# Optimization experiments

Hardware: AMD Instinct MI355X
Metric: run time of the kernel (lower is better)

## Reference

```python
import jax, jax.numpy as jnp
import numpy as np

N_NODES = 20000
N_EDGES = 320000
IN_DIM = 128
HID = 64
HEADS = 4
NEG_SLOPE = 0.2  # PyG GATConv default


def _glorot(key, shape):
    fan_in, fan_out = shape[0], shape[-1]
    lim = jnp.sqrt(6.0 / (fan_in + fan_out))
    return jax.random.uniform(key, shape, jnp.float32, -lim, lim)


def setup_inputs() -> dict:
    key = jax.random.key(0)
    ks = jax.random.split(key, 16)
    x = jax.random.normal(ks[0], (N_NODES, IN_DIM), jnp.float32)
    edge_index = jax.random.randint(ks[1], (2, N_EDGES), 0, N_NODES, dtype=jnp.int64)
    # layer 1: in=128 -> heads=4, out=64, concat
    W1 = _glorot(ks[2], (IN_DIM, HEADS * HID))
    a_src1 = _glorot(ks[3], (HEADS, HID))
    a_dst1 = _glorot(ks[4], (HEADS, HID))
    b1 = jnp.zeros((HEADS * HID,), jnp.float32)
    # layer 2: in=256 -> heads=4, out=64, concat
    W2 = _glorot(ks[5], (HEADS * HID, HEADS * HID))
    a_src2 = _glorot(ks[6], (HEADS, HID))
    a_dst2 = _glorot(ks[7], (HEADS, HID))
    b2 = jnp.zeros((HEADS * HID,), jnp.float32)
    # layer 3: in=256 -> heads=1, out=1, mean (concat=False)
    W3 = _glorot(ks[8], (HEADS * HID, 1))
    a_src3 = _glorot(ks[9], (1, 1))
    a_dst3 = _glorot(ks[10], (1, 1))
    b3 = jnp.zeros((1,), jnp.float32)
    return {
        "x": x, "edge_index": edge_index,
        "W1": W1, "a_src1": a_src1, "a_dst1": a_dst1, "b1": b1,
        "W2": W2, "a_src2": a_src2, "a_dst2": a_dst2, "b2": b2,
        "W3": W3, "a_src3": a_src3, "a_dst3": a_dst3, "b3": b3,
    }


def gat_conv(x, src, dst, W, a_src, a_dst, b, heads, out_c, concat):
    """PyG GATConv (add_self_loops already applied to src/dst)."""
    n = x.shape[0]
    h = (x @ W).reshape(n, heads, out_c)            # [N,H,C]
    alpha_s = jnp.sum(h * a_src, axis=-1)           # [N,H]
    alpha_d = jnp.sum(h * a_dst, axis=-1)           # [N,H]
    e = jax.nn.leaky_relu(alpha_s[src] + alpha_d[dst], NEG_SLOPE)  # [E,H]
    # segment softmax over incoming edges of each destination node
    e_max = jax.ops.segment_max(e, dst, num_segments=n)            # [N,H]
    ex = jnp.exp(e - e_max[dst])                                   # [E,H]
    denom = jax.ops.segment_sum(ex, dst, num_segments=n)           # [N,H]
    alpha = ex / denom[dst]                                        # [E,H]
    msg = h[src] * alpha[:, :, None]                               # [E,H,C]
    out = jax.ops.segment_sum(msg, dst, num_segments=n)            # [N,H,C]
    if concat:
        out = out.reshape(n, heads * out_c)
    else:
        out = out.mean(axis=1)
    return out + b


def reference(x, edge_index, W1, a_src1, a_dst1, b1, W2, a_src2, a_dst2, b2,
              W3, a_src3, a_dst3, b3):
    n = x.shape[0]
    loops = jnp.arange(n, dtype=edge_index.dtype)
    src = jnp.concatenate([edge_index[0], loops])
    dst = jnp.concatenate([edge_index[1], loops])
    h = jax.nn.elu(gat_conv(x, src, dst, W1, a_src1, a_dst1, b1, HEADS, HID, True))
    # dropout is identity in eval mode
    h = jax.nn.elu(gat_conv(h, src, dst, W2, a_src2, a_dst2, b2, HEADS, HID, True))
    h = gat_conv(h, src, dst, W3, a_src3, a_dst3, b3, 1, 1, False)
    return h.reshape(-1)
```

## Files before the change

kernel.cpp:

```cpp
#include <hip/hip_runtime.h>
#include <hip/hip_bf16.h>
#include <cmath>

#define N_NODESC 20000
#define E_RAW    320000
#define E_TOTC   340000
#define HEADSC   4
#define FC       256
#define NEG_SLOPE 0.2f
#define MAXD     512

typedef __attribute__((ext_vector_type(8))) short short8v;
typedef __attribute__((ext_vector_type(4))) float f32x4;

__device__ __forceinline__ int dstOf(const int* ei, int e) {
  return (e < E_RAW) ? ei[E_RAW + e] : (e - E_RAW);
}
__device__ __forceinline__ int srcOf(const int* ei, int e) {
  return (e < E_RAW) ? ei[e] : (e - E_RAW);
}
__device__ __forceinline__ float lrelu(float v) { return v > 0.f ? v : NEG_SLOPE * v; }

__device__ __forceinline__ unsigned short f2bf(float f) {
  __hip_bfloat16 h = __float2bfloat16(f);
  return reinterpret_cast<unsigned short&>(h);
}
__device__ __forceinline__ float bf2f(unsigned short u) {
  return __uint_as_float(((unsigned int)u) << 16);
}

__global__ void mega_prep(const float* __restrict__ x,
                          unsigned short* __restrict__ xhi, unsigned short* __restrict__ xlo,
                          const float* __restrict__ W1,
                          unsigned short* __restrict__ w1hi, unsigned short* __restrict__ w1lo,
                          const float* __restrict__ W2,
                          unsigned short* __restrict__ w2hi, unsigned short* __restrict__ w2lo,
                          int* __restrict__ deg) {
  const int bid = blockIdx.x, t = threadIdx.x;
  if (bid < 10000) {
    int i = bid * 256 + t;
    float v = x[i];
    unsigned short hh = f2bf(v);
    xhi[i] = hh; xlo[i] = f2bf(v - bf2f(hh));
  } else if (bid < 10128) {
    int idx = (bid - 10000) * 256 + t;
    int c = idx >> 7, k = idx & 127;
    float v = W1[k * FC + c];
    unsigned short hh = f2bf(v);
    w1hi[c * 128 + k] = hh; w1lo[c * 128 + k] = f2bf(v - bf2f(hh));
  } else if (bid < 10384) {
    int idx = (bid - 10128) * 256 + t;
    int c = idx >> 8, k = idx & 255;
    float v = W2[k * FC + c];
    unsigned short hh = f2bf(v);
    w2hi[c * 256 + k] = hh; w2lo[c * 256 + k] = f2bf(v - bf2f(hh));
  } else {
    int i = (bid - 10384) * 256 + t;
    if (i < N_NODESC) deg[i] = 0;
  }
}

template<int K>
__global__ void __launch_bounds__(256) mfma_gemm(
    const unsigned short* __restrict__ Ahi, const unsigned short* __restrict__ Alo,
    const unsigned short* __restrict__ WhiT, const unsigned short* __restrict__ WloT,
    const float* __restrict__ a_src, const float* __restrict__ a_dst,
    unsigned short* __restrict__ hb, float* __restrict__ as, float* __restrict__ ad) {
  __shared__ float asred[64][4];
  __shared__ float adred[64][4];
  const int t = threadIdx.x;
  const int w = t >> 6, l = t & 63;
  const int n0 = blockIdx.x * 64;
  const int r16 = l & 15;
  const int kq = l >> 4;
  const int col0 = w * 64;

  f32x4 acc[4][4];
#pragma unroll
  for (int rt = 0; rt < 4; ++rt)
#pragma unroll
    for (int ct = 0; ct < 4; ++ct) acc[rt][ct] = f32x4{0.f, 0.f, 0.f, 0.f};

  long arow[4];
#pragma unroll
  for (int rt = 0; rt < 4; ++rt) {
    int r = n0 + rt * 16 + r16;
    if (r >= N_NODESC) r = N_NODESC - 1;
    arow[rt] = (long)r * K;
  }

  for (int ks = 0; ks < K; ks += 32) {
    const int kb = ks + kq * 8;
    short8v aHi[4], aLo[4];
#pragma unroll
    for (int rt = 0; rt < 4; ++rt) {
      aHi[rt] = *(const short8v*)(Ahi + arow[rt] + kb);
      aLo[rt] = *(const short8v*)(Alo + arow[rt] + kb);
    }
#pragma unroll
    for (int ct = 0; ct < 4; ++ct) {
      const long wrow = (long)(col0 + ct * 16 + r16) * K + kb;
      short8v wHi = *(const short8v*)(WhiT + wrow);
      short8v wLo = *(const short8v*)(WloT + wrow);
#pragma unroll
      for (int rt = 0; rt < 4; ++rt) {
        acc[rt][ct] = __builtin_amdgcn_mfma_f32_16x16x32_bf16(aHi[rt], wHi, acc[rt][ct], 0, 0, 0);
        acc[rt][ct] = __builtin_amdgcn_mfma_f32_16x16x32_bf16(aHi[rt], wLo, acc[rt][ct], 0, 0, 0);
        acc[rt][ct] = __builtin_amdgcn_mfma_f32_16x16x32_bf16(aLo[rt], wHi, acc[rt][ct], 0, 0, 0);
      }
    }
  }

  float asv[4], adv[4];
#pragma unroll
  for (int ct = 0; ct < 4; ++ct) {
    int c = col0 + ct * 16 + r16;
    asv[ct] = a_src[c];
    adv[ct] = a_dst[c];
  }
#pragma unroll
  for (int rt = 0; rt < 4; ++rt) {
#pragma unroll
    for (int j = 0; j < 4; ++j) {
      const int r = rt * 16 + kq * 4 + j;
      const int g = n0 + r;
      if (g < N_NODESC) {
#pragma unroll
        for (int ct = 0; ct < 4; ++ct)
          hb[(long)g * FC + col0 + ct * 16 + r16] = f2bf(acc[rt][ct][j]);
      }
      float ps = acc[rt][0][j] * asv[0] + acc[rt][1][j] * asv[1]
               + acc[rt][2][j] * asv[2] + acc[rt][3][j] * asv[3];
      float pd = acc[rt][0][j] * adv[0] + acc[rt][1][j] * adv[1]
               + acc[rt][2][j] * adv[2] + acc[rt][3][j] * adv[3];
      for (int off = 8; off; off >>= 1) {
        ps += __shfl_down(ps, off, 16);
        pd += __shfl_down(pd, off, 16);
      }
      if (r16 == 0) {
        asred[r][w] = ps;
        adred[r][w] = pd;
      }
    }
  }
  __syncthreads();
  {
    const int rr = t >> 2, hh = t & 3;
    const int g = n0 + rr;
    if (g < N_NODESC) {
      as[(long)g * HEADSC + hh] = asred[rr][hh];
      ad[(long)g * HEADSC + hh] = adred[rr][hh];
    }
  }
}

__global__ void gemm3_kernel(const unsigned short* __restrict__ act_hi,
                             const unsigned short* __restrict__ act_lo,
                             const float* __restrict__ W3,
                             const float* __restrict__ asc, const float* __restrict__ adc,
                             float* __restrict__ h3, float* __restrict__ as,
                             float* __restrict__ ad) {
  const int n = blockIdx.x;
  const int t = threadIdx.x;
  float a = bf2f(act_hi[(long)n * FC + t]) + bf2f(act_lo[(long)n * FC + t]);
  float v = a * W3[t];
  for (int off = 32; off; off >>= 1) v += __shfl_down(v, off, 64);
  __shared__ float red[4];
  if ((t & 63) == 0) red[t >> 6] = v;
  __syncthreads();
  if (t == 0) {
    float s = red[0] + red[1] + red[2] + red[3];
    h3[n] = s;
    as[n] = s * asc[0];
    ad[n] = s * adc[0];
  }
}

__global__ void deg_count(const int* __restrict__ ei, int* __restrict__ deg) {
  int e = blockIdx.x * 256 + threadIdx.x;
  if (e >= E_TOTC) return;
  atomicAdd(&deg[dstOf(ei, e)], 1);
}

__global__ void scan_kernel(const int* __restrict__ deg, int* __restrict__ row_ptr,
                            int* __restrict__ cursor) {
  __shared__ int partial[1024];
  const int t = threadIdx.x;
  const int PER = (N_NODESC + 1023) / 1024;
  const int base = t * PER;
  int s = 0;
  for (int i = 0; i < PER; ++i) {
    int idx = base + i;
    if (idx < N_NODESC) s += deg[idx];
  }
  partial[t] = s;
  __syncthreads();
  for (int off = 1; off < 1024; off <<= 1) {
    int v = (t >= off) ? partial[t - off] : 0;
    __syncthreads();
    partial[t] += v;
    __syncthreads();
  }
  int run = (t == 0) ? 0 : partial[t - 1];
  for (int i = 0; i < PER; ++i) {
    int idx = base + i;
    if (idx < N_NODESC) {
      row_ptr[idx] = run;
      cursor[idx]  = run;
      run += deg[idx];
    }
  }
  if (t == 1023) row_ptr[N_NODESC] = run;
}

__global__ void fill_kernel(const int* __restrict__ ei, int* __restrict__ cursor,
                            int* __restrict__ col_src) {
  int e = blockIdx.x * 256 + threadIdx.x;
  if (e >= E_TOTC) return;
  int d = dstOf(ei, e);
  int pos = atomicAdd(&cursor[d], 1);
  col_src[pos] = srcOf(ei, e);
}

template<bool ELU>
__global__ void __launch_bounds__(128) fused_sa(
    const int* __restrict__ row_ptr, const int* __restrict__ col_src,
    const float4* __restrict__ as4, const float4* __restrict__ ad4,
    const unsigned short* __restrict__ hb, const float* __restrict__ b,
    unsigned short* __restrict__ out_hi, unsigned short* __restrict__ out_lo) {
  const int d = blockIdx.x;
  const int t = threadIdx.x;
  const int l = t & 63, wv = t >> 6;
  const int j0 = row_ptr[d], j1 = row_ptr[d + 1];
  const int deg = j1 - j0;
  __shared__ float4 wbuf[MAXD];
  __shared__ float4 xred[2];
  const float4 adv = ad4[d];

  float4 mx = float4{-INFINITY, -INFINITY, -INFINITY, -INFINITY};
  for (int j = j0 + t; j < j1; j += 128) {
    float4 a = as4[col_src[j]];
    float4 v;
    v.x = lrelu(a.x + adv.x); v.y = lrelu(a.y + adv.y);
    v.z = lrelu(a.z + adv.z); v.w = lrelu(a.w + adv.w);
    int jj = j - j0;
    if (jj < MAXD) wbuf[jj] = v;
    mx.x = fmaxf(mx.x, v.x); mx.y = fmaxf(mx.y, v.y);
    mx.z = fmaxf(mx.z, v.z); mx.w = fmaxf(mx.w, v.w);
  }
  for (int off = 32; off; off >>= 1) {
    mx.x = fmaxf(mx.x, __shfl_xor(mx.x, off, 64));
    mx.y = fmaxf(mx.y, __shfl_xor(mx.y, off, 64));
    mx.z = fmaxf(mx.z, __shfl_xor(mx.z, off, 64));
    mx.w = fmaxf(mx.w, __shfl_xor(mx.w, off, 64));
  }
  if (l == 0) xred[wv] = mx;
  __syncthreads();
  {
    float4 m0 = xred[0], m1 = xred[1];
    mx.x = fmaxf(m0.x, m1.x); mx.y = fmaxf(m0.y, m1.y);
    mx.z = fmaxf(m0.z, m1.z); mx.w = fmaxf(m0.w, m1.w);
  }
  __syncthreads();

  float4 sm = float4{0.f, 0.f, 0.f, 0.f};
  for (int j = j0 + t; j < j1; j += 128) {
    int jj = j - j0;
    float4 v;
    if (jj < MAXD) v = wbuf[jj];
    else {
      float4 a = as4[col_src[j]];
      v.x = lrelu(a.x + adv.x); v.y = lrelu(a.y + adv.y);
      v.z = lrelu(a.z + adv.z); v.w = lrelu(a.w + adv.w);
    }
    float4 e;
    e.x = expf(v.x - mx.x); e.y = expf(v.y - mx.y);
    e.z = expf(v.z - mx.z); e.w = expf(v.w - mx.w);
    if (jj < MAXD) wbuf[jj] = e;
    sm.x += e.x; sm.y += e.y; sm.z += e.z; sm.w += e.w;
  }
  for (int off = 32; off; off >>= 1) {
    sm.x += __shfl_xor(sm.x, off, 64);
    sm.y += __shfl_xor(sm.y, off, 64);
    sm.z += __shfl_xor(sm.z, off, 64);
    sm.w += __shfl_xor(sm.w, off, 64);
  }
  if (l == 0) xred[wv] = sm;
  __syncthreads();

  const int h = t >> 5;
  float st0, mxh, advh;
  {
    float4 s0 = xred[0], s1 = xred[1];
    float sx = s0.x + s1.x, sy = s0.y + s1.y, sz = s0.z + s1.z, sw = s0.w + s1.w;
    st0  = (h == 0) ? sx : (h == 1) ? sy : (h == 2) ? sz : sw;
    mxh  = (h == 0) ? mx.x : (h == 1) ? mx.y : (h == 2) ? mx.z : mx.w;
    advh = (h == 0) ? adv.x : (h == 1) ? adv.y : (h == 2) ? adv.z : adv.w;
  }
  const float dnh = 1.f / st0;

  const float* wlds = (const float*)wbuf;
  const ushort2* hb2 = (const ushort2*)hb;
  float a0 = 0.f, a1 = 0.f;
  if (deg <= MAXD) {
    int j = j0;
    for (; j + 8 <= j1; j += 8) {
      int     s[8];
      ushort2 v[8];
      float   w[8];
#pragma unroll
      for (int u = 0; u < 8; ++u) s[u] = col_src[j + u];
#pragma unroll
      for (int u = 0; u < 8; ++u) v[u] = hb2[(long)s[u] * 128 + t];
#pragma unroll
      for (int u = 0; u < 8; ++u) w[u] = wlds[(j + u - j0) * 4 + h];
#pragma unroll
      for (int u = 0; u < 8; ++u) {
        a0 = fmaf(w[u], bf2f(v[u].x), a0);
        a1 = fmaf(w[u], bf2f(v[u].y), a1);
      }
    }
    for (; j < j1; ++j) {
      ushort2 v = hb2[(long)col_src[j] * 128 + t];
      float w = wlds[(j - j0) * 4 + h];
      a0 = fmaf(w, bf2f(v.x), a0);
      a1 = fmaf(w, bf2f(v.y), a1);
    }
  } else {
    const float* asf = (const float*)as4;
    for (int j = j0; j < j1; ++j) {
      int s = col_src[j];
      float e = expf(lrelu(asf[s * 4 + h] + advh) - mxh);
      ushort2 v = hb2[(long)s * 128 + t];
      a0 = fmaf(e, bf2f(v.x), a0);
      a1 = fmaf(e, bf2f(v.y), a1);
    }
  }
  float o0 = a0 * dnh + b[2 * t];
  float o1 = a1 * dnh + b[2 * t + 1];
  if (ELU) {
    o0 = o0 > 0.f ? o0 : expm1f(o0);
    o1 = o1 > 0.f ? o1 : expm1f(o1);
  }
  ushort2 hi, lo;
  hi.x = f2bf(o0); lo.x = f2bf(o0 - bf2f(hi.x));
  hi.y = f2bf(o1); lo.y = f2bf(o1 - bf2f(hi.y));
  ((ushort2*)out_hi)[(long)d * 128 + t] = hi;
  ((ushort2*)out_lo)[(long)d * 128 + t] = lo;
}

__global__ void __launch_bounds__(256) fused_sa3(
    const int* __restrict__ row_ptr, const int* __restrict__ col_src,
    const float* __restrict__ as, const float* __restrict__ ad,
    const float* __restrict__ h3, const float* __restrict__ b3,
    float* __restrict__ out) {
  const int wv = threadIdx.x >> 6, l = threadIdx.x & 63;
  const int d = blockIdx.x * 4 + wv;
  if (d >= N_NODESC) return;
  const int j0 = row_ptr[d], j1 = row_ptr[d + 1];
  const float adv = ad[d];
  float mx = -INFINITY;
  for (int j = j0 + l; j < j1; j += 64)
    mx = fmaxf(mx, lrelu(as[col_src[j]] + adv));
  for (int off = 32; off; off >>= 1) mx = fmaxf(mx, __shfl_xor(mx, off, 64));
  float sm = 0.f, acc = 0.f;
  for (int j = j0 + l; j < j1; j += 64) {
    int s = col_src[j];
    float e = expf(lrelu(as[s] + adv) - mx);
    sm += e;
    acc = fmaf(e, h3[s], acc);
  }
  for (int off = 32; off; off >>= 1) {
    sm  += __shfl_xor(sm, off, 64);
    acc += __shfl_xor(acc, off, 64);
  }
  if (l == 0) out[d] = acc / sm + b3[0];
}

extern "C" void kernel_launch(void* const* d_in, const int* in_sizes, int n_in,
                              void* d_out, int out_size, void* d_ws, size_t ws_size,
                              hipStream_t stream) {
  const float* x    = (const float*)d_in[0];
  const int*   ei   = (const int*)d_in[1];
  const float* W1   = (const float*)d_in[2];
  const float* as1  = (const float*)d_in[3];
  const float* ad1  = (const float*)d_in[4];
  const float* b1   = (const float*)d_in[5];
  const float* W2   = (const float*)d_in[6];
  const float* as2  = (const float*)d_in[7];
  const float* ad2  = (const float*)d_in[8];
  const float* b2   = (const float*)d_in[9];
  const float* W3   = (const float*)d_in[10];
  const float* as3  = (const float*)d_in[11];
  const float* ad3  = (const float*)d_in[12];
  const float* b3   = (const float*)d_in[13];
  float* out = (float*)d_out;

  float* ws = (float*)d_ws;
  size_t off = 0;
  float* wAs   = ws + off; off += (size_t)N_NODESC * HEADSC;
  float* wAd   = ws + off; off += (size_t)N_NODESC * HEADSC;
  float* h3    = ws + off; off += N_NODESC;
  int* deg     = (int*)(ws + off); off += N_NODESC;
  int* row_ptr = (int*)(ws + off); off += N_NODESC + 1;
  int* cursor  = (int*)(ws + off); off += N_NODESC;
  int* col_src = (int*)(ws + off); off += E_TOTC;
  off = (off + 3) & ~(size_t)3;
  unsigned short* hb     = (unsigned short*)(ws + off); off += (size_t)N_NODESC * 128;
  unsigned short* act_hi = (unsigned short*)(ws + off); off += (size_t)N_NODESC * 128;
  unsigned short* act_lo = (unsigned short*)(ws + off); off += (size_t)N_NODESC * 128;
  unsigned short* xhi    = (unsigned short*)(ws + off); off += (size_t)N_NODESC * 64;
  unsigned short* xlo    = (unsigned short*)(ws + off); off += (size_t)N_NODESC * 64;
  unsigned short* W1hiT  = (unsigned short*)(ws + off); off += 16384;
  unsigned short* W1loT  = (unsigned short*)(ws + off); off += 16384;
  unsigned short* W2hiT  = (unsigned short*)(ws + off); off += 32768;
  unsigned short* W2loT  = (unsigned short*)(ws + off); off += 32768;

  const int gridE  = (E_TOTC + 255) / 256;
  const int gridN4 = (N_NODESC + 3) / 4;
  const int gemmG  = (N_NODESC + 63) / 64;

  mega_prep<<<10463, 256, 0, stream>>>(x, xhi, xlo, W1, W1hiT, W1loT,
                                       W2, W2hiT, W2loT, deg);
  deg_count<<<gridE, 256, 0, stream>>>(ei, deg);
  scan_kernel<<<1, 1024, 0, stream>>>(deg, row_ptr, cursor);
  fill_kernel<<<gridE, 256, 0, stream>>>(ei, cursor, col_src);

  mfma_gemm<128><<<gemmG, 256, 0, stream>>>(xhi, xlo, W1hiT, W1loT, as1, ad1, hb, wAs, wAd);
  fused_sa<true><<<N_NODESC, 128, 0, stream>>>(row_ptr, col_src, (const float4*)wAs,
                                               (const float4*)wAd, hb, b1, act_hi, act_lo);

  mfma_gemm<256><<<gemmG, 256, 0, stream>>>(act_hi, act_lo, W2hiT, W2loT, as2, ad2, hb, wAs, wAd);
  fused_sa<true><<<N_NODESC, 128, 0, stream>>>(row_ptr, col_src, (const float4*)wAs,
                                               (const float4*)wAd, hb, b2, act_hi, act_lo);

  gemm3_kernel<<<N_NODESC, 256, 0, stream>>>(act_hi, act_lo, W3, as3, ad3, h3, wAs, wAd);
  fused_sa3<<<gridN4, 256, 0, stream>>>(row_ptr, col_src, wAs, wAd, h3, b3, out);
}
```

Baseline: 234.2 us.

## Fuse layer-3 projection into layer-2 aggregation and use wave-shuffle scan

The layer-2 aggregation kernel now computes the layer-3 dot product with W3 directly from its fp32 outputs and writes h3 and the attention scalars. This removes the separate gemm3 launch and the write and re-read of the hi/lo bf16 activation buffers. The single-block scan also replaces its LDS Hillis-Steele loop, which synchronised on every step, with wave shuffles plus a small per-wave offset pass. In exchange, the fused kernel gains an extra reduction and a __syncthreads at its tail.

```diff
diff --git a/kernel.cpp b/kernel.cpp
--- a/kernel.cpp
+++ b/kernel.cpp
@@ -154,28 +154,6 @@
   }
 }
 
-__global__ void gemm3_kernel(const unsigned short* __restrict__ act_hi,
-                             const unsigned short* __restrict__ act_lo,
-                             const float* __restrict__ W3,
-                             const float* __restrict__ asc, const float* __restrict__ adc,
-                             float* __restrict__ h3, float* __restrict__ as,
-                             float* __restrict__ ad) {
-  const int n = blockIdx.x;
-  const int t = threadIdx.x;
-  float a = bf2f(act_hi[(long)n * FC + t]) + bf2f(act_lo[(long)n * FC + t]);
-  float v = a * W3[t];
-  for (int off = 32; off; off >>= 1) v += __shfl_down(v, off, 64);
-  __shared__ float red[4];
-  if ((t & 63) == 0) red[t >> 6] = v;
-  __syncthreads();
-  if (t == 0) {
-    float s = red[0] + red[1] + red[2] + red[3];
-    h3[n] = s;
-    as[n] = s * asc[0];
-    ad[n] = s * adc[0];
-  }
-}
-
 __global__ void deg_count(const int* __restrict__ ei, int* __restrict__ deg) {
   int e = blockIdx.x * 256 + threadIdx.x;
   if (e >= E_TOTC) return;
@@ -184,24 +162,29 @@
 
 __global__ void scan_kernel(const int* __restrict__ deg, int* __restrict__ row_ptr,
                             int* __restrict__ cursor) {
-  __shared__ int partial[1024];
   const int t = threadIdx.x;
+  const int lane = t & 63, wid = t >> 6;
   const int PER = (N_NODESC + 1023) / 1024;
   const int base = t * PER;
-  int s = 0;
+  int own = 0;
   for (int i = 0; i < PER; ++i) {
     int idx = base + i;
-    if (idx < N_NODESC) s += deg[idx];
-  }
-  partial[t] = s;
-  __syncthreads();
-  for (int off = 1; off < 1024; off <<= 1) {
-    int v = (t >= off) ? partial[t - off] : 0;
-    __syncthreads();
-    partial[t] += v;
-    __syncthreads();
-  }
-  int run = (t == 0) ? 0 : partial[t - 1];
+    if (idx < N_NODESC) own += deg[idx];
+  }
+  int inc = own;
+  for (int off = 1; off < 64; off <<= 1) {
+    int v = __shfl_up(inc, off, 64);
+    if (lane >= off) inc += v;
+  }
+  __shared__ int wtot[16], woff[16];
+  if (lane == 63) wtot[wid] = inc;
+  __syncthreads();
+  if (t == 0) {
+    int r = 0;
+    for (int i = 0; i < 16; ++i) { woff[i] = r; r += wtot[i]; }
+  }
+  __syncthreads();
+  int run = woff[wid] + inc - own;
   for (int i = 0; i < PER; ++i) {
     int idx = base + i;
     if (idx < N_NODESC) {
@@ -222,12 +205,15 @@
   col_src[pos] = srcOf(ei, e);
 }
 
-template<bool ELU>
+template<int MODE>
 __global__ void __launch_bounds__(128) fused_sa(
     const int* __restrict__ row_ptr, const int* __restrict__ col_src,
     const float4* __restrict__ as4, const float4* __restrict__ ad4,
     const unsigned short* __restrict__ hb, const float* __restrict__ b,
-    unsigned short* __restrict__ out_hi, unsigned short* __restrict__ out_lo) {
+    unsigned short* __restrict__ out_hi, unsigned short* __restrict__ out_lo,
+    const float* __restrict__ W3, const float* __restrict__ asc3,
+    const float* __restrict__ adc3, float* __restrict__ h3,
+    float* __restrict__ a3s, float* __restrict__ a3d) {
   const int d = blockIdx.x;
   const int t = threadIdx.x;
   const int l = t & 63, wv = t >> 6;
@@ -338,15 +324,28 @@
   }
   float o0 = a0 * dnh + b[2 * t];
   float o1 = a1 * dnh + b[2 * t + 1];
-  if (ELU) {
-    o0 = o0 > 0.f ? o0 : expm1f(o0);
-    o1 = o1 > 0.f ? o1 : expm1f(o1);
-  }
-  ushort2 hi, lo;
-  hi.x = f2bf(o0); lo.x = f2bf(o0 - bf2f(hi.x));
-  hi.y = f2bf(o1); lo.y = f2bf(o1 - bf2f(hi.y));
-  ((ushort2*)out_hi)[(long)d * 128 + t] = hi;
-  ((ushort2*)out_lo)[(long)d * 128 + t] = lo;
+  o0 = o0 > 0.f ? o0 : expm1f(o0);
+  o1 = o1 > 0.f ? o1 : expm1f(o1);
+
+  if (MODE == 0) {
+    ushort2 hi, lo;
+    hi.x = f2bf(o0); lo.x = f2bf(o0 - bf2f(hi.x));
+    hi.y = f2bf(o1); lo.y = f2bf(o1 - bf2f(hi.y));
+    ((ushort2*)out_hi)[(long)d * 128 + t] = hi;
+    ((ushort2*)out_lo)[(long)d * 128 + t] = lo;
+  } else {
+    float p = o0 * W3[2 * t] + o1 * W3[2 * t + 1];
+    for (int off = 32; off; off >>= 1) p += __shfl_down(p, off, 64);
+    __shared__ float pred[2];
+    if (l == 0) pred[wv] = p;
+    __syncthreads();
+    if (t == 0) {
+      float s = pred[0] + pred[1];
+      h3[d]  = s;
+      a3s[d] = s * asc3[0];
+      a3d[d] = s * adc3[0];
+    }
+  }
 }
 
 __global__ void __launch_bounds__(256) fused_sa3(
@@ -401,6 +400,8 @@
   float* wAs   = ws + off; off += (size_t)N_NODESC * HEADSC;
   float* wAd   = ws + off; off += (size_t)N_NODESC * HEADSC;
   float* h3    = ws + off; off += N_NODESC;
+  float* a3s   = ws + off; off += N_NODESC;
+  float* a3d   = ws + off; off += N_NODESC;
   int* deg     = (int*)(ws + off); off += N_NODESC;
   int* row_ptr = (int*)(ws + off); off += N_NODESC + 1;
   int* cursor  = (int*)(ws + off); off += N_NODESC;
@@ -427,13 +428,14 @@
   fill_kernel<<<gridE, 256, 0, stream>>>(ei, cursor, col_src);
 
   mfma_gemm<128><<<gemmG, 256, 0, stream>>>(xhi, xlo, W1hiT, W1loT, as1, ad1, hb, wAs, wAd);
-  fused_sa<true><<<N_NODESC, 128, 0, stream>>>(row_ptr, col_src, (const float4*)wAs,
-                                               (const float4*)wAd, hb, b1, act_hi, act_lo);
+  fused_sa<0><<<N_NODESC, 128, 0, stream>>>(row_ptr, col_src, (const float4*)wAs,
+                                            (const float4*)wAd, hb, b1, act_hi, act_lo,
+                                            nullptr, nullptr, nullptr, nullptr, nullptr, nullptr);
 
   mfma_gemm<256><<<gemmG, 256, 0, stream>>>(act_hi, act_lo, W2hiT, W2loT, as2, ad2, hb, wAs, wAd);
-  fused_sa<true><<<N_NODESC, 128, 0, stream>>>(row_ptr, col_src, (const float4*)wAs,
-                                               (const float4*)wAd, hb, b2, act_hi, act_lo);
-
-  gemm3_kernel<<<N_NODESC, 256, 0, stream>>>(act_hi, act_lo, W3, as3, ad3, h3, wAs, wAd);
-  fused_sa3<<<gridN4, 256, 0, stream>>>(row_ptr, col_src, wAs, wAd, h3, b3, out);
-}
+  fused_sa<1><<<N_NODESC, 128, 0, stream>>>(row_ptr, col_src, (const float4*)wAs,
+                                            (const float4*)wAd, hb, b2, nullptr, nullptr,
+                                            W3, as3, ad3, h3, a3s, a3d);
+
+  fused_sa3<<<gridN4, 256, 0, stream>>>(row_ptr, col_src, a3s, a3d, h3, b3, out);
+}
```

Measured after the change: 233.1 us. About the same (-0.4%).
